# Kernel tuning notes

Measured on AMD Instinct MI355X. Metric: run time of the kernel, lower is better.

The kernel has to match this reference:

```python
import jax, jax.numpy as jnp
import numpy as np

FP8_MAX = 448.0  # torch.finfo(float8_e4m3fn).max
BLK = 128
EPS = 1e-12

def fp8_round(x):
    # saturated cast to float8_e4m3fn and back (emulates to_fp8_saturated)
    y = jnp.clip(x, -FP8_MAX, FP8_MAX)
    return y.astype(jnp.float8_e4m3fn).astype(jnp.float32)

def per_tile_quant_dequant(x):
    # activation: 1x128 tiles along the feature dim
    S, D = x.shape
    t = x.reshape(S, D // BLK, BLK)
    amax = jnp.max(jnp.abs(t), axis=-1, keepdims=True)
    scale = jnp.maximum(amax, EPS) / FP8_MAX
    q = fp8_round(t / scale)
    return (q * scale).reshape(S, D)

def per_block_quant_dequant_weight(w):
    # weight: 128x128 blocks, w is [ne, dout, din]
    ne, do, di = w.shape
    blk = w.reshape(ne, do // BLK, BLK, di // BLK, BLK)
    amax = jnp.max(jnp.abs(blk), axis=(2, 4), keepdims=True)
    scale = jnp.maximum(amax, EPS) / FP8_MAX
    q = fp8_round(blk / scale)
    return (q * scale).reshape(ne, do, di)

def setup_inputs() -> dict:
    key = jax.random.key(0)
    k1, k2 = jax.random.split(key)
    NE, DOUT, DIN, SEQ = 8, 1024, 2048, 16384
    x = jax.random.normal(k1, (SEQ, DIN), dtype=jnp.float32)
    w = jax.random.normal(k2, (NE * DOUT, DIN), dtype=jnp.float32) * 0.02
    tokens_per_expert = jnp.full((NE,), SEQ // NE, dtype=jnp.int32)
    return {"input": x, "tokens_per_expert": tokens_per_expert, "weight": w}

def reference(input, tokens_per_expert, weight):
    NE = tokens_per_expert.shape[0]
    S, DIN = input.shape
    DOUT = weight.shape[0] // NE
    w = weight.reshape(NE, DOUT, DIN)
    w_dq = per_block_quant_dequant_weight(w)   # fp8 per-block weight, dequantized
    x_dq = per_tile_quant_dequant(input)       # fp8 per-tile activation, dequantized
    # grouped varlen GEMM; tokens are split equally across experts here
    T = S // NE
    xe = x_dq.reshape(NE, T, DIN)
    out = jnp.einsum('etd,eod->eto', xe, w_dq)  # [ne, T, dout]
    return out.reshape(S, DOUT)
```

## Files before the change

kernel.cpp:

```cpp
#include <hip/hip_runtime.h>
#include <hip/hip_bf16.h>
#include <hip/hip_fp8.h>

#define SEQ   16384
#define DIN_  2048
#define DOUT_ 1024
#define NE_   8
#define TPE   (SEQ / NE_)
#define NT    (DIN_ / 64)

typedef __bf16 bf16x8 __attribute__((ext_vector_type(8)));
typedef __bf16 bf16x4 __attribute__((ext_vector_type(4)));
typedef float  f32x4  __attribute__((ext_vector_type(4)));

#define GLD(gp, lp) __builtin_amdgcn_global_load_lds( \
    (const __attribute__((address_space(1))) unsigned int*)(gp), \
    (__attribute__((address_space(3))) unsigned int*)(lp), 16, 0, 0)

__device__ __forceinline__ float fp8_round_dq_m(float v, float sinv, float s) {
    float r = v * sinv;
    r = fminf(fmaxf(r, -448.0f), 448.0f);
    __hip_fp8_e4m3 q(r);
    return (float)q * s;
}

__global__ __launch_bounds__(256) void quant_x_kernel(const float* __restrict__ X,
                                                      __bf16* __restrict__ Xq) {
    const int t    = threadIdx.x;
    const int lane = t & 63;
    const int wave = t >> 6;
    const int tile = wave * 4 + (lane >> 4);
    const int sub  = lane & 15;
    const size_t off = (size_t)tile * 128 + sub * 8;

    const int row0 = blockIdx.x * 2;
    const float* pa = X + (size_t)row0 * DIN_ + off;
    const float* pb = X + (size_t)(row0 + 1) * DIN_ + off;

    float4 a0 = *(const float4*)pa;
    float4 a1 = *(const float4*)(pa + 4);
    float4 b0 = *(const float4*)pb;
    float4 b1 = *(const float4*)(pb + 4);

    float ma = fmaxf(fmaxf(fmaxf(fabsf(a0.x), fabsf(a0.y)), fmaxf(fabsf(a0.z), fabsf(a0.w))),
                     fmaxf(fmaxf(fabsf(a1.x), fabsf(a1.y)), fmaxf(fabsf(a1.z), fabsf(a1.w))));
    float mb = fmaxf(fmaxf(fmaxf(fabsf(b0.x), fabsf(b0.y)), fmaxf(fabsf(b0.z), fabsf(b0.w))),
                     fmaxf(fmaxf(fabsf(b1.x), fabsf(b1.y)), fmaxf(fabsf(b1.z), fabsf(b1.w))));
    #pragma unroll
    for (int off2 = 1; off2 < 16; off2 <<= 1) {
        ma = fmaxf(ma, __shfl_xor(ma, off2, 64));
        mb = fmaxf(mb, __shfl_xor(mb, off2, 64));
    }

    const float sa = fmaxf(ma, 1e-12f) / 448.0f, sia = 1.0f / sa;
    const float sb = fmaxf(mb, 1e-12f) / 448.0f, sib = 1.0f / sb;

    bf16x8 oa, ob;
    oa[0] = (__bf16)fp8_round_dq_m(a0.x, sia, sa);
    oa[1] = (__bf16)fp8_round_dq_m(a0.y, sia, sa);
    oa[2] = (__bf16)fp8_round_dq_m(a0.z, sia, sa);
    oa[3] = (__bf16)fp8_round_dq_m(a0.w, sia, sa);
    oa[4] = (__bf16)fp8_round_dq_m(a1.x, sia, sa);
    oa[5] = (__bf16)fp8_round_dq_m(a1.y, sia, sa);
    oa[6] = (__bf16)fp8_round_dq_m(a1.z, sia, sa);
    oa[7] = (__bf16)fp8_round_dq_m(a1.w, sia, sa);
    ob[0] = (__bf16)fp8_round_dq_m(b0.x, sib, sb);
    ob[1] = (__bf16)fp8_round_dq_m(b0.y, sib, sb);
    ob[2] = (__bf16)fp8_round_dq_m(b0.z, sib, sb);
    ob[3] = (__bf16)fp8_round_dq_m(b0.w, sib, sb);
    ob[4] = (__bf16)fp8_round_dq_m(b1.x, sib, sb);
    ob[5] = (__bf16)fp8_round_dq_m(b1.y, sib, sb);
    ob[6] = (__bf16)fp8_round_dq_m(b1.z, sib, sb);
    ob[7] = (__bf16)fp8_round_dq_m(b1.w, sib, sb);
    *(bf16x8*)(Xq + (size_t)row0 * DIN_ + off) = oa;
    *(bf16x8*)(Xq + (size_t)(row0 + 1) * DIN_ + off) = ob;
}

__global__ __launch_bounds__(256) void quant_w_kernel(const float* __restrict__ W,
                                                      __bf16* __restrict__ Wq) {
    const int rb = blockIdx.x >> 4;
    const int cb = blockIdx.x & 15;
    const int t  = threadIdx.x;

    const float* base = W + (size_t)(rb * 128) * DIN_ + cb * 128;
    const int r0 = t >> 5;
    const int c0 = (t & 31) * 4;

    float4 v[16];
    float m = 0.0f;
    #pragma unroll
    for (int i = 0; i < 16; ++i) {
        v[i] = *(const float4*)(base + (size_t)(i * 8 + r0) * DIN_ + c0);
        m = fmaxf(m, fmaxf(fmaxf(fabsf(v[i].x), fabsf(v[i].y)),
                           fmaxf(fabsf(v[i].z), fabsf(v[i].w))));
    }
    #pragma unroll
    for (int off = 1; off < 64; off <<= 1)
        m = fmaxf(m, __shfl_xor(m, off, 64));
    __shared__ float smx[4];
    if ((t & 63) == 0) smx[t >> 6] = m;
    __syncthreads();
    const float amax = fmaxf(fmaxf(smx[0], smx[1]), fmaxf(smx[2], smx[3]));
    const float s    = fmaxf(amax, 1e-12f) / 448.0f;
    const float sinv = 1.0f / s;

    __bf16* obase = Wq + (size_t)(rb * 128) * DIN_ + cb * 128;
    #pragma unroll
    for (int i = 0; i < 16; ++i) {
        bf16x4 o;
        o[0] = (__bf16)fp8_round_dq_m(v[i].x, sinv, s);
        o[1] = (__bf16)fp8_round_dq_m(v[i].y, sinv, s);
        o[2] = (__bf16)fp8_round_dq_m(v[i].z, sinv, s);
        o[3] = (__bf16)fp8_round_dq_m(v[i].w, sinv, s);
        *(bf16x4*)(obase + (size_t)(i * 8 + r0) * DIN_ + c0) = o;
    }
}

__global__ __launch_bounds__(512, 2) void gemm_kernel(const __bf16* __restrict__ X,
                                                      const __bf16* __restrict__ W,
                                                      float* __restrict__ out) {
    __shared__ __align__(16) unsigned char lds[131072];

    const int bid  = blockIdx.x;
    const int wgid = (bid & 7) * 32 + (bid >> 3);
    const int e    = wgid >> 5;
    const int tile = wgid & 31;
    const int brow = tile >> 2;
    const int bcol = tile & 3;

    const int t     = threadIdx.x;
    const int lane  = t & 63;
    const int wave  = t >> 6;
    const int wm    = wave >> 2;
    const int wn    = wave & 3;
    const int flane = lane & 15;

    const __bf16* Xt = X + (size_t)(e * TPE + brow * 256) * DIN_;
    const __bf16* Wt = W + (size_t)(e * DOUT_ + bcol * 256) * DIN_;

    auto stage = [&](int j, bool isA, int kh) {
        if (j >= NT) return;
        const int buf = j & 1;
        const unsigned base = (isA ? 0u : 65536u) + (unsigned)(buf * 2 + kh) * 16384u;
        const __bf16* src = isA ? Xt : Wt;
        #pragma unroll
        for (int i = 0; i < 2; ++i) {
            const unsigned p = (unsigned)i * 8192u + (unsigned)t * 16u;
            const unsigned q = p ^ (((p >> 7) & 3u) << 4);
            GLD(src + (size_t)(q >> 6) * DIN_ + j * 64 + kh * 32 + ((q & 63u) >> 1),
                &lds[base + p]);
        }
    };

    auto ldf = [&](unsigned base, int row) -> bf16x8 {
        unsigned p = (unsigned)row * 64u + (unsigned)(lane >> 4) * 16u;
        p ^= ((p >> 7) & 3u) << 4;
        return *(const bf16x8*)&lds[base + p];
    };

    bf16x8 aA[4], aB[4], b0[4], b1[4];
    f32x4 acc[8][4] = {};

    #define ABASE(buf, kh) ((unsigned)((buf) * 2 + (kh)) * 16384u)
    #define BBASE(buf, kh) (65536u + (unsigned)((buf) * 2 + (kh)) * 16384u)
    #define PRE_A(dst, buf, kh, m0) \
        { _Pragma("unroll") for (int m_ = 0; m_ < 4; ++m_) \
            dst[m_] = ldf(ABASE(buf, kh), wm * 128 + ((m0) + m_) * 16 + flane); }
    #define PRE_B(dst, buf, kh) \
        { _Pragma("unroll") for (int n_ = 0; n_ < 4; ++n_) \
            dst[n_] = ldf(BBASE(buf, kh), wn * 64 + n_ * 16 + flane); }
    #define MFMA4x4(alo, aset, bset) \
        { _Pragma("unroll") for (int m_ = 0; m_ < 4; ++m_) \
            _Pragma("unroll") for (int n_ = 0; n_ < 4; ++n_) \
                acc[(alo) + m_][n_] = __builtin_amdgcn_mfma_f32_16x16x32_bf16( \
                    aset[m_], bset[n_], acc[(alo) + m_][n_], 0, 0, 0); }

    stage(0, false, 0); stage(0, false, 1); stage(0, true, 0);
    stage(0, true, 1);  stage(1, false, 0); stage(1, false, 1); stage(1, true, 0);
    asm volatile("s_waitcnt vmcnt(8)" ::: "memory");
    __builtin_amdgcn_s_barrier();
    PRE_A(aA, 0, 0, 0);
    PRE_B(b0, 0, 0);

    for (int kt = 0; kt < NT; ++kt) {
        const int buf = kt & 1;

        PRE_A(aB, buf, 0, 4);
        stage(kt + 1, true, 1);
        asm volatile("s_waitcnt lgkmcnt(4)" ::: "memory");
        __builtin_amdgcn_sched_barrier(0);
        __builtin_amdgcn_s_setprio(1);
        MFMA4x4(0, aA, b0);
        __builtin_amdgcn_s_setprio(0);
        if (kt < NT - 1) asm volatile("s_waitcnt vmcnt(8)" ::: "memory");
        else             asm volatile("s_waitcnt vmcnt(0)" ::: "memory");
        __builtin_amdgcn_s_barrier();

        PRE_A(aA, buf, 1, 0);
        PRE_B(b1, buf, 1);
        stage(kt + 2, false, 0);
        asm volatile("s_waitcnt lgkmcnt(8)" ::: "memory");
        __builtin_amdgcn_sched_barrier(0);
        __builtin_amdgcn_s_setprio(1);
        MFMA4x4(4, aB, b0);
        __builtin_amdgcn_s_setprio(0);
        __builtin_amdgcn_s_barrier();

        PRE_A(aB, buf, 1, 4);
        asm volatile("s_waitcnt lgkmcnt(4)" ::: "memory");
        __builtin_amdgcn_sched_barrier(0);
        __builtin_amdgcn_s_setprio(1);
        MFMA4x4(0, aA, b1);
        __builtin_amdgcn_s_setprio(0);
        if (kt < NT - 2)      asm volatile("s_waitcnt vmcnt(4)" ::: "memory");
        else if (kt == NT - 2) asm volatile("s_waitcnt vmcnt(2)" ::: "memory");
        __builtin_amdgcn_s_barrier();

        if (kt < NT - 1) {
            PRE_A(aA, buf ^ 1, 0, 0);
            PRE_B(b0, buf ^ 1, 0);
        }
        stage(kt + 2, false, 1);
        stage(kt + 2, true, 0);
        if (kt < NT - 1) asm volatile("s_waitcnt lgkmcnt(8)" ::: "memory");
        else             asm volatile("s_waitcnt lgkmcnt(0)" ::: "memory");
        __builtin_amdgcn_sched_barrier(0);
        __builtin_amdgcn_s_setprio(1);
        MFMA4x4(4, aB, b1);
        __builtin_amdgcn_s_setprio(0);
        __builtin_amdgcn_s_barrier();
    }

    const int orow0 = e * TPE + brow * 256 + wm * 128;
    const int ocol0 = bcol * 256 + wn * 64;
    const int rl = (lane >> 4) * 4;
    const int cl = lane & 15;
    #pragma unroll
    for (int m = 0; m < 8; ++m)
        #pragma unroll
        for (int n = 0; n < 4; ++n)
            #pragma unroll
            for (int j = 0; j < 4; ++j) {
                const int r = orow0 + m * 16 + rl + j;
                const int c = ocol0 + n * 16 + cl;
                out[(size_t)r * DOUT_ + c] = acc[m][n][j];
            }
}

extern "C" void kernel_launch(void* const* d_in, const int* in_sizes, int n_in,
                              void* d_out, int out_size, void* d_ws, size_t ws_size,
                              hipStream_t stream) {
    const float* x = (const float*)d_in[0];
    const float* w = (const float*)d_in[2];
    float* out = (float*)d_out;

    __bf16* xq = (__bf16*)d_ws;
    __bf16* wq = (__bf16*)((char*)d_ws + (size_t)SEQ * DIN_ * sizeof(__bf16));

    quant_x_kernel<<<SEQ / 2, 256, 0, stream>>>(x, xq);
    quant_w_kernel<<<(NE_ * DOUT_ / 128) * (DIN_ / 128), 256, 0, stream>>>(w, wq);
    gemm_kernel<<<NE_ * (TPE / 256) * (DOUT_ / 256), 512, 0, stream>>>(xq, wq, out);
}
```

Baseline: 121.5 us.

## Restructure GEMM LDS staging to full-K tiles and quantize four rows per block

```diff
diff --git a/kernel.cpp b/kernel.cpp
--- a/kernel.cpp
+++ b/kernel.cpp
@@ -33,47 +33,40 @@
     const int sub  = lane & 15;
     const size_t off = (size_t)tile * 128 + sub * 8;
 
-    const int row0 = blockIdx.x * 2;
-    const float* pa = X + (size_t)row0 * DIN_ + off;
-    const float* pb = X + (size_t)(row0 + 1) * DIN_ + off;
-
-    float4 a0 = *(const float4*)pa;
-    float4 a1 = *(const float4*)(pa + 4);
-    float4 b0 = *(const float4*)pb;
-    float4 b1 = *(const float4*)(pb + 4);
-
-    float ma = fmaxf(fmaxf(fmaxf(fabsf(a0.x), fabsf(a0.y)), fmaxf(fabsf(a0.z), fabsf(a0.w))),
-                     fmaxf(fmaxf(fabsf(a1.x), fabsf(a1.y)), fmaxf(fabsf(a1.z), fabsf(a1.w))));
-    float mb = fmaxf(fmaxf(fmaxf(fabsf(b0.x), fabsf(b0.y)), fmaxf(fabsf(b0.z), fabsf(b0.w))),
-                     fmaxf(fmaxf(fabsf(b1.x), fabsf(b1.y)), fmaxf(fabsf(b1.z), fabsf(b1.w))));
-    #pragma unroll
-    for (int off2 = 1; off2 < 16; off2 <<= 1) {
-        ma = fmaxf(ma, __shfl_xor(ma, off2, 64));
-        mb = fmaxf(mb, __shfl_xor(mb, off2, 64));
-    }
-
-    const float sa = fmaxf(ma, 1e-12f) / 448.0f, sia = 1.0f / sa;
-    const float sb = fmaxf(mb, 1e-12f) / 448.0f, sib = 1.0f / sb;
-
-    bf16x8 oa, ob;
-    oa[0] = (__bf16)fp8_round_dq_m(a0.x, sia, sa);
-    oa[1] = (__bf16)fp8_round_dq_m(a0.y, sia, sa);
-    oa[2] = (__bf16)fp8_round_dq_m(a0.z, sia, sa);
-    oa[3] = (__bf16)fp8_round_dq_m(a0.w, sia, sa);
-    oa[4] = (__bf16)fp8_round_dq_m(a1.x, sia, sa);
-    oa[5] = (__bf16)fp8_round_dq_m(a1.y, sia, sa);
-    oa[6] = (__bf16)fp8_round_dq_m(a1.z, sia, sa);
-    oa[7] = (__bf16)fp8_round_dq_m(a1.w, sia, sa);
-    ob[0] = (__bf16)fp8_round_dq_m(b0.x, sib, sb);
-    ob[1] = (__bf16)fp8_round_dq_m(b0.y, sib, sb);
-    ob[2] = (__bf16)fp8_round_dq_m(b0.z, sib, sb);
-    ob[3] = (__bf16)fp8_round_dq_m(b0.w, sib, sb);
-    ob[4] = (__bf16)fp8_round_dq_m(b1.x, sib, sb);
-    ob[5] = (__bf16)fp8_round_dq_m(b1.y, sib, sb);
-    ob[6] = (__bf16)fp8_round_dq_m(b1.z, sib, sb);
-    ob[7] = (__bf16)fp8_round_dq_m(b1.w, sib, sb);
-    *(bf16x8*)(Xq + (size_t)row0 * DIN_ + off) = oa;
-    *(bf16x8*)(Xq + (size_t)(row0 + 1) * DIN_ + off) = ob;
+    const int row0 = blockIdx.x * 4;
+    float4 v0[4], v1[4];
+    float mx[4];
+    #pragma unroll
+    for (int r = 0; r < 4; ++r) {
+        const float* p = X + (size_t)(row0 + r) * DIN_ + off;
+        v0[r] = *(const float4*)p;
+        v1[r] = *(const float4*)(p + 4);
+        mx[r] = fmaxf(fmaxf(fmaxf(fabsf(v0[r].x), fabsf(v0[r].y)),
+                            fmaxf(fabsf(v0[r].z), fabsf(v0[r].w))),
+                      fmaxf(fmaxf(fabsf(v1[r].x), fabsf(v1[r].y)),
+                            fmaxf(fabsf(v1[r].z), fabsf(v1[r].w))));
+    }
+    #pragma unroll
+    for (int o = 1; o < 16; o <<= 1) {
+        #pragma unroll
+        for (int r = 0; r < 4; ++r)
+            mx[r] = fmaxf(mx[r], __shfl_xor(mx[r], o, 64));
+    }
+    #pragma unroll
+    for (int r = 0; r < 4; ++r) {
+        const float s    = fmaxf(mx[r], 1e-12f) / 448.0f;
+        const float sinv = 1.0f / s;
+        bf16x8 o;
+        o[0] = (__bf16)fp8_round_dq_m(v0[r].x, sinv, s);
+        o[1] = (__bf16)fp8_round_dq_m(v0[r].y, sinv, s);
+        o[2] = (__bf16)fp8_round_dq_m(v0[r].z, sinv, s);
+        o[3] = (__bf16)fp8_round_dq_m(v0[r].w, sinv, s);
+        o[4] = (__bf16)fp8_round_dq_m(v1[r].x, sinv, s);
+        o[5] = (__bf16)fp8_round_dq_m(v1[r].y, sinv, s);
+        o[6] = (__bf16)fp8_round_dq_m(v1[r].z, sinv, s);
+        o[7] = (__bf16)fp8_round_dq_m(v1[r].w, sinv, s);
+        *(bf16x8*)(Xq + (size_t)(row0 + r) * DIN_ + off) = o;
+    }
 }
 
 __global__ __launch_bounds__(256) void quant_w_kernel(const float* __restrict__ W,
@@ -138,45 +131,43 @@
     const __bf16* Xt = X + (size_t)(e * TPE + brow * 256) * DIN_;
     const __bf16* Wt = W + (size_t)(e * DOUT_ + bcol * 256) * DIN_;
 
-    auto stage = [&](int j, bool isA, int kh) {
+    auto stage = [&](int j, bool isA) {
         if (j >= NT) return;
-        const int buf = j & 1;
-        const unsigned base = (isA ? 0u : 65536u) + (unsigned)(buf * 2 + kh) * 16384u;
+        const unsigned base = (isA ? 0u : 65536u) + (unsigned)(j & 1) * 32768u;
         const __bf16* src = isA ? Xt : Wt;
         #pragma unroll
-        for (int i = 0; i < 2; ++i) {
+        for (int i = 0; i < 4; ++i) {
             const unsigned p = (unsigned)i * 8192u + (unsigned)t * 16u;
-            const unsigned q = p ^ (((p >> 7) & 3u) << 4);
-            GLD(src + (size_t)(q >> 6) * DIN_ + j * 64 + kh * 32 + ((q & 63u) >> 1),
+            const unsigned q = p ^ (((p >> 7) & 7u) << 4);
+            GLD(src + (size_t)(q >> 7) * DIN_ + j * 64 + ((q & 127u) >> 1),
                 &lds[base + p]);
         }
     };
 
-    auto ldf = [&](unsigned base, int row) -> bf16x8 {
-        unsigned p = (unsigned)row * 64u + (unsigned)(lane >> 4) * 16u;
-        p ^= ((p >> 7) & 3u) << 4;
+    auto ldf = [&](unsigned base, int row, int kh) -> bf16x8 {
+        unsigned p = (unsigned)row * 128u + (unsigned)kh * 64u + (unsigned)(lane >> 4) * 16u;
+        p ^= ((p >> 7) & 7u) << 4;
         return *(const bf16x8*)&lds[base + p];
     };
 
     bf16x8 aA[4], aB[4], b0[4], b1[4];
     f32x4 acc[8][4] = {};
 
-    #define ABASE(buf, kh) ((unsigned)((buf) * 2 + (kh)) * 16384u)
-    #define BBASE(buf, kh) (65536u + (unsigned)((buf) * 2 + (kh)) * 16384u)
+    #define ABASE(buf) ((unsigned)(buf) * 32768u)
+    #define BBASE(buf) (65536u + (unsigned)(buf) * 32768u)
     #define PRE_A(dst, buf, kh, m0) \
         { _Pragma("unroll") for (int m_ = 0; m_ < 4; ++m_) \
-            dst[m_] = ldf(ABASE(buf, kh), wm * 128 + ((m0) + m_) * 16 + flane); }
+            dst[m_] = ldf(ABASE(buf), wm * 128 + ((m0) + m_) * 16 + flane, kh); }
     #define PRE_B(dst, buf, kh) \
         { _Pragma("unroll") for (int n_ = 0; n_ < 4; ++n_) \
-            dst[n_] = ldf(BBASE(buf, kh), wn * 64 + n_ * 16 + flane); }
+            dst[n_] = ldf(BBASE(buf), wn * 64 + n_ * 16 + flane, kh); }
     #define MFMA4x4(alo, aset, bset) \
         { _Pragma("unroll") for (int m_ = 0; m_ < 4; ++m_) \
             _Pragma("unroll") for (int n_ = 0; n_ < 4; ++n_) \
                 acc[(alo) + m_][n_] = __builtin_amdgcn_mfma_f32_16x16x32_bf16( \
                     aset[m_], bset[n_], acc[(alo) + m_][n_], 0, 0, 0); }
 
-    stage(0, false, 0); stage(0, false, 1); stage(0, true, 0);
-    stage(0, true, 1);  stage(1, false, 0); stage(1, false, 1); stage(1, true, 0);
+    stage(0, false); stage(0, true); stage(1, false); stage(1, true);
     asm volatile("s_waitcnt vmcnt(8)" ::: "memory");
     __builtin_amdgcn_s_barrier();
     PRE_A(aA, 0, 0, 0);
@@ -186,19 +177,15 @@
         const int buf = kt & 1;
 
         PRE_A(aB, buf, 0, 4);
-        stage(kt + 1, true, 1);
         asm volatile("s_waitcnt lgkmcnt(4)" ::: "memory");
         __builtin_amdgcn_sched_barrier(0);
         __builtin_amdgcn_s_setprio(1);
         MFMA4x4(0, aA, b0);
         __builtin_amdgcn_s_setprio(0);
-        if (kt < NT - 1) asm volatile("s_waitcnt vmcnt(8)" ::: "memory");
-        else             asm volatile("s_waitcnt vmcnt(0)" ::: "memory");
         __builtin_amdgcn_s_barrier();
 
         PRE_A(aA, buf, 1, 0);
         PRE_B(b1, buf, 1);
-        stage(kt + 2, false, 0);
         asm volatile("s_waitcnt lgkmcnt(8)" ::: "memory");
         __builtin_amdgcn_sched_barrier(0);
         __builtin_amdgcn_s_setprio(1);
@@ -209,22 +196,22 @@
         PRE_A(aB, buf, 1, 4);
         asm volatile("s_waitcnt lgkmcnt(4)" ::: "memory");
         __builtin_amdgcn_sched_barrier(0);
+        stage(kt + 2, false);
         __builtin_amdgcn_s_setprio(1);
         MFMA4x4(0, aA, b1);
         __builtin_amdgcn_s_setprio(0);
-        if (kt < NT - 2)      asm volatile("s_waitcnt vmcnt(4)" ::: "memory");
-        else if (kt == NT - 2) asm volatile("s_waitcnt vmcnt(2)" ::: "memory");
+        if (kt < NT - 2) asm volatile("s_waitcnt vmcnt(4)" ::: "memory");
+        else             asm volatile("s_waitcnt vmcnt(0)" ::: "memory");
         __builtin_amdgcn_s_barrier();
 
         if (kt < NT - 1) {
             PRE_A(aA, buf ^ 1, 0, 0);
             PRE_B(b0, buf ^ 1, 0);
         }
-        stage(kt + 2, false, 1);
-        stage(kt + 2, true, 0);
         if (kt < NT - 1) asm volatile("s_waitcnt lgkmcnt(8)" ::: "memory");
         else             asm volatile("s_waitcnt lgkmcnt(0)" ::: "memory");
         __builtin_amdgcn_sched_barrier(0);
+        stage(kt + 2, true);
         __builtin_amdgcn_s_setprio(1);
         MFMA4x4(4, aB, b1);
         __builtin_amdgcn_s_setprio(0);
@@ -257,7 +244,7 @@
     __bf16* xq = (__bf16*)d_ws;
     __bf16* wq = (__bf16*)((char*)d_ws + (size_t)SEQ * DIN_ * sizeof(__bf16));
 
-    quant_x_kernel<<<SEQ / 2, 256, 0, stream>>>(x, xq);
+    quant_x_kernel<<<SEQ / 4, 256, 0, stream>>>(x, xq);
     quant_w_kernel<<<(NE_ * DOUT_ / 128) * (DIN_ / 128), 256, 0, stream>>>(w, wq);
     gemm_kernel<<<NE_ * (TPE / 256) * (DOUT_ / 256), 512, 0, stream>>>(xq, wq, out);
 }
```

Result: no change. 121.9 us (+0.3%).
